# Performance work log

Hardware: AMD Instinct MI355X
Metric: run time of the kernel (lower is better)

Reference implementation:

```python
import jax, jax.numpy as jnp
import numpy as np

H = 16      # num_attention_heads
D = 128     # head_size
ROT = 32    # rotary_ndims
WIN = 256   # attention_window[layer_id]
G = 64      # max_global_tokens
BASE = 10000.0


def _rotate_half(x):
    x1, x2 = jnp.split(x, 2, axis=-1)
    return jnp.concatenate([-x2, x1], axis=-1)


def setup_inputs() -> dict:
    key = jax.random.key(0)
    ks = jax.random.split(key, 6)
    B, S, HD = 2, 2048, H * D
    hidden_states = jax.random.normal(ks[0], (B, S, HD), jnp.float32)
    attention_mask = jnp.zeros((B, 1, 1, S), jnp.float32)
    glob_idx = jnp.sort(jax.random.randint(ks[1], (B, G), 0, S), axis=-1)
    W_qkv = jax.random.normal(ks[2], (HD, 3 * HD), jnp.float32) * 0.02
    b_qkv = jnp.zeros((3 * HD,), jnp.float32)
    W_o = jax.random.normal(ks[3], (HD, HD), jnp.float32) * 0.02
    b_o = jnp.zeros((HD,), jnp.float32)
    return {"hidden_states": hidden_states, "attention_mask": attention_mask,
            "glob_idx": glob_idx, "W_qkv": W_qkv, "b_qkv": b_qkv,
            "W_o": W_o, "b_o": b_o}


def reference(hidden_states, attention_mask, glob_idx, W_qkv, b_qkv, W_o, b_o):
    B, S, HD = hidden_states.shape
    qkv = (hidden_states @ W_qkv + b_qkv).reshape(B, S, H, 3 * D)
    q = qkv[..., :D].transpose(0, 2, 1, 3)        # [B,H,S,D]
    k = qkv[..., D:2 * D].transpose(0, 2, 1, 3)
    v = qkv[..., 2 * D:].transpose(0, 2, 1, 3)

    # GPT-NeoX rotary on first ROT dims
    inv_freq = 1.0 / (BASE ** (jnp.arange(0, ROT, 2, dtype=jnp.float32) / ROT))
    freqs = jnp.einsum('s,f->sf', jnp.arange(S, dtype=jnp.float32), inv_freq)
    emb = jnp.concatenate([freqs, freqs], axis=-1)           # [S,ROT]
    cos = jnp.cos(emb)[None, None]
    sin = jnp.sin(emb)[None, None]
    q = jnp.concatenate([q[..., :ROT] * cos + _rotate_half(q[..., :ROT]) * sin,
                         q[..., ROT:]], axis=-1)
    k = jnp.concatenate([k[..., :ROT] * cos + _rotate_half(k[..., :ROT]) * sin,
                         k[..., ROT:]], axis=-1)

    # step_attn path: keys/values are head-averaged before attention (key.mean(1))
    k_mean = k.mean(axis=1)   # [B,S,D]
    v_mean = v.mean(axis=1)
    scale = 1.0 / jnp.sqrt(jnp.float32(D))
    minv = jnp.finfo(jnp.float32).min

    s0 = jnp.einsum('bhqd,bkd->bhqk', q[:, :, :WIN], k_mean[:, :WIN]) * scale
    causal = jnp.tril(jnp.ones((WIN, WIN), bool))
    s0 = jnp.where(causal[None, None], s0, minv) + attention_mask[..., :WIN]
    out0 = jnp.einsum('bhqk,bkd->bhqd', jax.nn.softmax(s0, axis=-1), v_mean[:, :WIN])

    Sq = S - WIN
    steps = jnp.arange(Sq)
    win_pos = steps[:, None] + 1 + jnp.arange(WIN)[None, :]
    k_win = k_mean[:, win_pos]
    v_win = v_mean[:, win_pos]
    mask_win = attention_mask[:, 0, 0, :][:, win_pos][:, None]
    qs = q[:, :, WIN:]                                        # [B,H,Sq,D]
    s_win = jnp.einsum('bhqd,bqwd->bhqw', qs, k_win) * scale + mask_win

    k_glob = jnp.take_along_axis(k_mean, glob_idx[..., None], axis=1)  # [B,G,D]
    v_glob = jnp.take_along_axis(v_mean, glob_idx[..., None], axis=1)
    # sorted indices: 'filter < i then truncate to G' == prefix-valid mask per slot
    valid = (glob_idx[:, None, :] < steps[None, :, None])[:, None]     # [B,1,Sq,G]
    s_glob = jnp.where(valid, jnp.einsum('bhqd,bgd->bhqg', qs, k_glob) * scale, minv)

    w = jax.nn.softmax(jnp.concatenate([s_glob, s_win], axis=-1), axis=-1)
    out_steps = (jnp.einsum('bhqg,bgd->bhqd', w[..., :G], v_glob)
                 + jnp.einsum('bhqw,bqwd->bhqd', w[..., G:], v_win))

    out = jnp.concatenate([out0, out_steps], axis=2)          # [B,H,S,D]
    out = out.transpose(0, 2, 1, 3).reshape(B, S, HD)
    return out @ W_o + b_o
```

## Files before the change

### kernel.cpp

```cpp
#include <hip/hip_runtime.h>
#include <math.h>

#define SCALE_ 0.08838834764831845f
#define MINV_  (-3.4028234663852886e38f)

typedef __bf16 bf16;
typedef bf16  bf16x4 __attribute__((ext_vector_type(4)));
typedef bf16  bf16x8 __attribute__((ext_vector_type(8)));
typedef float f32x4  __attribute__((ext_vector_type(4)));
typedef float f32x16 __attribute__((ext_vector_type(16)));
typedef float float4v __attribute__((ext_vector_type(4)));

#define LD8(p) (*(const bf16x8*)(p))

__device__ __forceinline__ f32x4 mfma16(bf16x8 a, bf16x8 b, f32x4 c) {
    return __builtin_amdgcn_mfma_f32_16x16x32_bf16(a, b, c, 0, 0, 0);
}
__device__ __forceinline__ f32x16 mfma32(bf16x8 a, bf16x8 b, f32x16 c) {
    return __builtin_amdgcn_mfma_f32_32x32x16_bf16(a, b, c, 0, 0, 0);
}

typedef const __attribute__((address_space(1))) void* gas_t;
typedef __attribute__((address_space(3))) void* sas_t;
__device__ __forceinline__ void gload_lds16(const void* g, void* l) {
    __builtin_amdgcn_global_load_lds((gas_t)g, (sas_t)l, 16, 0, 0);
}

__global__ __launch_bounds__(256) void prep_kernel(const float* __restrict__ hidden, bf16* __restrict__ A16,
                                                   const float* __restrict__ Wqkv, bf16* __restrict__ BT1,
                                                   const float* __restrict__ Wo, bf16* __restrict__ BT2,
                                                   const float* __restrict__ bqkv, float* __restrict__ bias1)
{
    int x = blockIdx.x;
    if (x < 512) {
        int k0 = x * 4;
        int j = threadIdx.x;
        float acc[4];
        #pragma unroll
        for (int k = 0; k < 4; k++) acc[k] = 0.f;
        for (int h = 0; h < 16; h++) {
            #pragma unroll
            for (int k = 0; k < 4; k++)
                acc[k] += Wqkv[(size_t)(k0 + k) * 6144 + h * 384 + 128 + j];
        }
        #pragma unroll
        for (int k = 0; k < 4; k++)
            BT1[(size_t)(2048 + j) * 2048 + k0 + k] = (bf16)(acc[k] * 0.0625f);
        return;
    }
    if (x == 512) {
        for (int c = threadIdx.x; c < 2304; c += 256) {
            if (c < 2048) bias1[c] = bqkv[(c >> 7) * 384 + (c & 127)];
            else {
                int j = c - 2048; float s = 0.f;
                for (int h = 0; h < 16; h++) s += bqkv[h * 384 + 128 + j];
                bias1[c] = s * 0.0625f;
            }
        }
        return;
    }
    if (x < 8705) {
        int i = ((x - 513) * 256 + threadIdx.x) * 4;
        float4v v = *(const float4v*)(hidden + i);
        bf16x4 o; o.x = (bf16)v.x; o.y = (bf16)v.y; o.z = (bf16)v.z; o.w = (bf16)v.w;
        *(bf16x4*)(A16 + i) = o;
        return;
    }
    __shared__ float tile[32][33];
    int t = x - 8705;
    int z = t >> 12;
    int tt = t & 4095;
    const float* W = z ? Wo : Wqkv;
    bf16* BT = z ? BT2 : BT1;
    int srcStride = z ? 2048 : 6144;
    int k0 = (tt & 63) * 32, n0 = (tt >> 6) * 32;
    int c = threadIdx.x & 31, r = threadIdx.x >> 5;
    int n = n0 + c;
    int src = z ? n : ((n >> 7) * 384 + (n & 127));
    #pragma unroll
    for (int rr = 0; rr < 32; rr += 8)
        tile[r + rr][c] = W[(size_t)(k0 + r + rr) * srcStride + src];
    __syncthreads();
    #pragma unroll
    for (int rr = 0; rr < 32; rr += 8)
        BT[(size_t)(n0 + r + rr) * 2048 + k0 + c] = (bf16)tile[c][r + rr];
}


#define GEMM64_PROLOGUE_AND_KLOOP                                                         \
    __shared__ __align__(16) bf16 As[128 * 64];                                           \
    __shared__ __align__(16) bf16 Bs[64 * 64];                                            \
    const int tid  = threadIdx.x;                                                         \
    const int wv   = tid >> 6, lane = tid & 63, l32 = lane & 31, half = lane >> 5;        \
    const int m0 = blockIdx.y * 128, n0 = blockIdx.x * 64;                                \
    int rowSA[4], colSA[4];                                                               \
    _Pragma("unroll")                                                                     \
    for (int j = 0; j < 4; j++) {                                                         \
        int flat = (wv * 4 + j) * 64 + lane;                                              \
        rowSA[j] = flat >> 3;                                                             \
        colSA[j] = ((flat & 7) ^ (rowSA[j] & 7)) * 8;                                     \
    }                                                                                     \
    int rowSB[2], colSB[2];                                                               \
    _Pragma("unroll")                                                                     \
    for (int j = 0; j < 2; j++) {                                                         \
        int flat = (wv * 2 + j) * 64 + lane;                                              \
        rowSB[j] = flat >> 3;                                                             \
        colSB[j] = ((flat & 7) ^ (rowSB[j] & 7)) * 8;                                     \
    }                                                                                     \
    f32x16 acc[2];                                                                        \
    _Pragma("unroll")                                                                     \
    for (int i = 0; i < 2; i++)                                                           \
        _Pragma("unroll")                                                                 \
        for (int r = 0; r < 16; r++) acc[i][r] = 0.f;                                     \
    for (int kk = 0; kk < K; kk += 64) {                                                  \
        __syncthreads();                                                                  \
        _Pragma("unroll")                                                                 \
        for (int j = 0; j < 4; j++)                                                       \
            gload_lds16(A  + (size_t)(m0 + rowSA[j]) * K + kk + colSA[j], &As[(wv * 4 + j) * 512]); \
        _Pragma("unroll")                                                                 \
        for (int j = 0; j < 2; j++)                                                       \
            gload_lds16(BT + (size_t)(n0 + rowSB[j]) * K + kk + colSB[j], &Bs[(wv * 2 + j) * 512]); \
        __syncthreads();                                                                  \
        bf16x8 af[4], bfr[2][4];                                                          \
        const int rowA = wv * 32 + l32;                                                   \
        _Pragma("unroll")                                                                 \
        for (int k16 = 0; k16 < 4; k16++) {                                               \
            int lc = k16 * 2 + half;                                                      \
            af[k16] = LD8(&As[rowA * 64 + ((lc ^ (rowA & 7)) * 8)]);                      \
        }                                                                                 \
        _Pragma("unroll")                                                                 \
        for (int nt = 0; nt < 2; nt++) {                                                  \
            int rowB = nt * 32 + l32;                                                     \
            _Pragma("unroll")                                                             \
            for (int k16 = 0; k16 < 4; k16++) {                                           \
                int lc = k16 * 2 + half;                                                  \
                bfr[nt][k16] = LD8(&Bs[rowB * 64 + ((lc ^ (rowB & 7)) * 8)]);             \
            }                                                                             \
        }                                                                                 \
        _Pragma("unroll")                                                                 \
        for (int k16 = 0; k16 < 4; k16++)                                                 \
            _Pragma("unroll")                                                             \
            for (int nt = 0; nt < 2; nt++)                                                \
                acc[nt] = mfma32(af[k16], bfr[nt][k16], acc[nt]);                         \
    }

__global__ __launch_bounds__(256) void gemm_rot_kernel(const bf16* __restrict__ A, const bf16* __restrict__ BT,
                                                       const float* __restrict__ bias, bf16* __restrict__ C,
                                                       int M, int N, int K)
{
    GEMM64_PROLOGUE_AND_KLOOP

    #pragma unroll
    for (int nt = 0; nt < 2; nt++) {
        int n = n0 + nt * 32 + l32;
        float bn = bias[n];
        const bool rot = ((n0 & 127) == 0) && (nt == 0) && (n0 <= 2048);
        float inv = rot ? __expf(-0.575646273248511f * (float)(l32 & 15)) : 0.f;
        #pragma unroll
        for (int r = 0; r < 16; r++) {
            int m = m0 + wv * 32 + (r & 3) + 8 * (r >> 2) + 4 * half;
            float v = acc[nt][r] + bn;
            if (rot) {
                float ang = (float)(m & 2047) * inv;
                float cs, sn;
                __sincosf(ang, &sn, &cs);
                float pv = __shfl_xor(v, 16, 64);
                v = (l32 < 16) ? (v * cs - pv * sn) : (v * cs + pv * sn);
            }
            C[(size_t)m * N + n] = (bf16)v;
        }
    }
}

__global__ __launch_bounds__(256) void gemm_out_kernel(const bf16* __restrict__ A, const bf16* __restrict__ BT,
                                                       const float* __restrict__ bias, float* __restrict__ C,
                                                       int M, int N, int K)
{
    GEMM64_PROLOGUE_AND_KLOOP

    #pragma unroll
    for (int nt = 0; nt < 2; nt++) {
        int n = n0 + nt * 32 + l32;
        float bn = bias[n];
        #pragma unroll
        for (int r = 0; r < 16; r++) {
            int m = m0 + wv * 32 + (r & 3) + 8 * (r >> 2) + 4 * half;
            C[(size_t)m * N + n] = acc[nt][r] + bn;
        }
    }
}

__global__ __launch_bounds__(256) void pretile_kernel(const bf16* __restrict__ C1, const int* __restrict__ gidx,
                                                      bf16* __restrict__ KF, bf16* __restrict__ VF)
{
    __shared__ bf16 Vt[64][130];
    const int c = blockIdx.x, b = blockIdx.y;
    const bool isGlob = (c == 32);
    const int tid = threadIdx.x;

    {
        int row = tid >> 2, cb = (tid & 3) * 32;
        int pos = isGlob ? gidx[b * 64 + row] : (c * 64 + row);
        const bf16* src = C1 + (size_t)(b * 2048 + pos) * 2304 + 2176 + cb;
        #pragma unroll
        for (int k = 0; k < 4; k++)
            *(bf16x8*)&Vt[row][cb + k * 8] = LD8(src + k * 8);
    }
    __syncthreads();

    #pragma unroll
    for (int i = 0; i < 4; i++) {
        int sid = tid + i * 256;
        int lane = sid & 63, fi = sid >> 6;
        int l16 = lane & 15, quad = lane >> 4;
        int t = fi >> 2, ks = fi & 3;
        int pos = isGlob ? gidx[b * 64 + t * 16 + l16] : (c * 64 + t * 16 + l16);
        const bf16* src = C1 + (size_t)(b * 2048 + pos) * 2304 + 2048 + ks * 32 + quad * 8;
        *(bf16x8*)&KF[((size_t)(b * 33 + c) * 16 + fi) * 512 + lane * 8] = LD8(src);
    }

    #pragma unroll
    for (int i = 0; i < 4; i++) {
        int sid = tid + i * 256;
        int lane = sid & 63, fi = sid >> 6;
        int l16 = lane & 15, quad = lane >> 4;
        int dt = fi >> 1, ks2 = fi & 1;
        int d = dt * 16 + l16;
        bf16x8 v;
        #pragma unroll
        for (int j = 0; j < 8; j++)
            v[j] = Vt[ks2 * 32 + quad * 8 + j][d];
        *(bf16x8*)&VF[((size_t)(b * 33 + c) * 16 + fi) * 512 + lane * 8] = v;
    }
}

#define PSTRIDE 88

__device__ __forceinline__ void attn0_body(int bx, int h, int b, bf16* Pw,
                                           const bf16* __restrict__ C1, const bf16* __restrict__ KF,
                                           const bf16* __restrict__ VF, const float* __restrict__ mask,
                                           bf16* __restrict__ attn)
{
    const int tid = threadIdx.x, wv = tid >> 6, lane = tid & 63, quad = lane >> 4, l16 = lane & 15;
    const int q0 = (bx * 4 + wv) * 16;

    bf16x8 af[4];
    const bf16* qbase = C1 + (size_t)(b * 2048 + q0 + l16) * 2304 + h * 128;
    #pragma unroll
    for (int ks = 0; ks < 4; ks++) af[ks] = LD8(qbase + ks * 32 + quad * 8);

    f32x4 m_run = (f32x4){MINV_, MINV_, MINV_, MINV_};
    f32x4 l_run = (f32x4){0.f, 0.f, 0.f, 0.f};
    f32x4 O[8];
    #pragma unroll
    for (int dt = 0; dt < 8; dt++) O[dt] = (f32x4){0.f, 0.f, 0.f, 0.f};

    for (int c = 0; c <= bx; c++) {
        const bf16* KFc = KF + ((size_t)(b * 33 + c) * 16) * 512;
        const bf16* VFc = VF + ((size_t)(b * 33 + c) * 16) * 512;

        f32x4 acc[4];
        #pragma unroll
        for (int t = 0; t < 4; t++) acc[t] = (f32x4){0.f, 0.f, 0.f, 0.f};
        #pragma unroll
        for (int t = 0; t < 4; t++)
            #pragma unroll
            for (int ks = 0; ks < 4; ks++)
                acc[t] = mfma16(af[ks], LD8(KFc + (size_t)(t * 4 + ks) * 512 + lane * 8), acc[t]);

        float sv[4][4];
        #pragma unroll
        for (int t = 0; t < 4; t++) {
            int key = c * 64 + t * 16 + l16;
            float addv = mask[b * 2048 + key];
            #pragma unroll
            for (int r = 0; r < 4; r++) {
                int q = q0 + quad * 4 + r;
                sv[t][r] = (key <= q) ? (acc[t][r] * SCALE_ + addv) : MINV_;
            }
        }

        f32x4 cm;
        #pragma unroll
        for (int r = 0; r < 4; r++) cm[r] = fmaxf(fmaxf(sv[0][r], sv[1][r]), fmaxf(sv[2][r], sv[3][r]));
        #pragma unroll
        for (int ms = 1; ms < 16; ms <<= 1)
            #pragma unroll
            for (int r = 0; r < 4; r++) cm[r] = fmaxf(cm[r], __shfl_xor(cm[r], ms, 64));

        f32x4 nm, alpha;
        #pragma unroll
        for (int r = 0; r < 4; r++) { nm[r] = fmaxf(m_run[r], cm[r]); alpha[r] = __expf(m_run[r] - nm[r]); }

        float pv[4][4];
        f32x4 cs = (f32x4){0.f, 0.f, 0.f, 0.f};
        #pragma unroll
        for (int t = 0; t < 4; t++)
            #pragma unroll
            for (int r = 0; r < 4; r++) {
                pv[t][r] = __expf(sv[t][r] - nm[r]);
                cs[r] += pv[t][r];
            }
        #pragma unroll
        for (int ms = 1; ms < 16; ms <<= 1)
            #pragma unroll
            for (int r = 0; r < 4; r++) cs[r] += __shfl_xor(cs[r], ms, 64);

        m_run = nm;
        #pragma unroll
        for (int r = 0; r < 4; r++) l_run[r] = l_run[r] * alpha[r] + cs[r];
        #pragma unroll
        for (int dt = 0; dt < 8; dt++)
            #pragma unroll
            for (int r = 0; r < 4; r++) O[dt][r] *= alpha[r];

        #pragma unroll
        for (int t = 0; t < 4; t++)
            #pragma unroll
            for (int r = 0; r < 4; r++)
                Pw[(quad * 4 + r) * PSTRIDE + t * 16 + l16] = (bf16)pv[t][r];
        bf16x8 pa0 = LD8(&Pw[l16 * PSTRIDE + quad * 8]);
        bf16x8 pa1 = LD8(&Pw[l16 * PSTRIDE + 32 + quad * 8]);

        #pragma unroll
        for (int dt = 0; dt < 8; dt++) {
            O[dt] = mfma16(pa0, LD8(VFc + (size_t)(dt * 2 + 0) * 512 + lane * 8), O[dt]);
            O[dt] = mfma16(pa1, LD8(VFc + (size_t)(dt * 2 + 1) * 512 + lane * 8), O[dt]);
        }
    }

    f32x4 invl;
    #pragma unroll
    for (int r = 0; r < 4; r++) invl[r] = 1.0f / l_run[r];
    #pragma unroll
    for (int dt = 0; dt < 8; dt++)
        #pragma unroll
        for (int r = 0; r < 4; r++) {
            int q = q0 + quad * 4 + r;
            attn[(size_t)(b * 2048 + q) * 2048 + h * 128 + dt * 16 + l16] = (bf16)(O[dt][r] * invl[r]);
        }
}

__device__ __forceinline__ void attn_steps_body(int sb, int b, bf16* Pw,
                                                const bf16* __restrict__ C1, const bf16* __restrict__ KF,
                                                const bf16* __restrict__ VF, const float* __restrict__ mask,
                                                const int* __restrict__ gidx, bf16* __restrict__ attn)
{
    const int tid = threadIdx.x, wv = tid >> 6, lane = tid & 63, quad = lane >> 4, l16 = lane & 15;
    const int step = sb * 4 + wv, p = 256 + step;

    bf16x8 af[4];
    const bf16* qrow = C1 + (size_t)(b * 2048 + p) * 2304;
    #pragma unroll
    for (int ks = 0; ks < 4; ks++) af[ks] = LD8(qrow + l16 * 128 + ks * 32 + quad * 8);

    int gix[4];
    #pragma unroll
    for (int t = 0; t < 4; t++) gix[t] = gidx[b * 64 + t * 16 + l16];

    f32x4 m_run = (f32x4){MINV_, MINV_, MINV_, MINV_};
    f32x4 l_run = (f32x4){0.f, 0.f, 0.f, 0.f};
    f32x4 O[8];
    #pragma unroll
    for (int dt = 0; dt < 8; dt++) O[dt] = (f32x4){0.f, 0.f, 0.f, 0.f};

    const int c0 = (step + 1) >> 6;

    for (int iter = 0; iter < 6; iter++) {
        int c;
        bool isGlob = (iter == 0);
        if (isGlob) c = 32;
        else { c = c0 + iter - 1; if (c > 31) break; }

        const bf16* KFc = KF + ((size_t)(b * 33 + c) * 16) * 512;
        const bf16* VFc = VF + ((size_t)(b * 33 + c) * 16) * 512;

        f32x4 acc[4];
        #pragma unroll
        for (int t = 0; t < 4; t++) acc[t] = (f32x4){0.f, 0.f, 0.f, 0.f};
        #pragma unroll
        for (int t = 0; t < 4; t++)
            #pragma unroll
            for (int ks = 0; ks < 4; ks++)
                acc[t] = mfma16(af[ks], LD8(KFc + (size_t)(t * 4 + ks) * 512 + lane * 8), acc[t]);

        float sv[4][4];
        bool vld[4];
        #pragma unroll
        for (int t = 0; t < 4; t++) {
            float addv = 0.f;
            if (isGlob) vld[t] = gix[t] < step;
            else {
                int pos = c * 64 + t * 16 + l16;
                vld[t] = (unsigned)(pos - step - 1) < 256u;
                addv = mask[b * 2048 + pos];
            }
            #pragma unroll
            for (int r = 0; r < 4; r++) sv[t][r] = vld[t] ? (acc[t][r] * SCALE_ + addv) : MINV_;
        }

        f32x4 cm;
        #pragma unroll
        for (int r = 0; r < 4; r++) cm[r] = fmaxf(fmaxf(sv[0][r], sv[1][r]), fmaxf(sv[2][r], sv[3][r]));
        #pragma unroll
        for (int ms = 1; ms < 16; ms <<= 1)
            #pragma unroll
            for (int r = 0; r < 4; r++) cm[r] = fmaxf(cm[r], __shfl_xor(cm[r], ms, 64));

        f32x4 nm, alpha;
        #pragma unroll
        for (int r = 0; r < 4; r++) { nm[r] = fmaxf(m_run[r], cm[r]); alpha[r] = __expf(m_run[r] - nm[r]); }

        float pv[4][4];
        f32x4 cs = (f32x4){0.f, 0.f, 0.f, 0.f};
        #pragma unroll
        for (int t = 0; t < 4; t++)
            #pragma unroll
            for (int r = 0; r < 4; r++) {
                pv[t][r] = vld[t] ? __expf(sv[t][r] - nm[r]) : 0.f;
                cs[r] += pv[t][r];
            }
        #pragma unroll
        for (int ms = 1; ms < 16; ms <<= 1)
            #pragma unroll
            for (int r = 0; r < 4; r++) cs[r] += __shfl_xor(cs[r], ms, 64);

        m_run = nm;
        #pragma unroll
        for (int r = 0; r < 4; r++) l_run[r] = l_run[r] * alpha[r] + cs[r];
        #pragma unroll
        for (int dt = 0; dt < 8; dt++)
            #pragma unroll
            for (int r = 0; r < 4; r++) O[dt][r] *= alpha[r];

        #pragma unroll
        for (int t = 0; t < 4; t++)
            #pragma unroll
            for (int r = 0; r < 4; r++)
                Pw[(quad * 4 + r) * PSTRIDE + t * 16 + l16] = (bf16)pv[t][r];
        bf16x8 pa0 = LD8(&Pw[l16 * PSTRIDE + quad * 8]);
        bf16x8 pa1 = LD8(&Pw[l16 * PSTRIDE + 32 + quad * 8]);

        #pragma unroll
        for (int dt = 0; dt < 8; dt++) {
            O[dt] = mfma16(pa0, LD8(VFc + (size_t)(dt * 2 + 0) * 512 + lane * 8), O[dt]);
            O[dt] = mfma16(pa1, LD8(VFc + (size_t)(dt * 2 + 1) * 512 + lane * 8), O[dt]);
        }
    }

    f32x4 invl;
    #pragma unroll
    for (int r = 0; r < 4; r++) invl[r] = 1.0f / l_run[r];
    #pragma unroll
    for (int dt = 0; dt < 8; dt++)
        #pragma unroll
        for (int r = 0; r < 4; r++) {
            int h = quad * 4 + r;
            attn[(size_t)(b * 2048 + p) * 2048 + h * 128 + dt * 16 + l16] = (bf16)(O[dt][r] * invl[r]);
        }
}

__global__ __launch_bounds__(256) void attn_all_kernel(const bf16* __restrict__ C1, const bf16* __restrict__ KF,
                                                       const bf16* __restrict__ VF, const float* __restrict__ mask,
                                                       const int* __restrict__ gidx, bf16* __restrict__ attn)
{
    __shared__ __align__(16) bf16 Ps[4 * 16 * PSTRIDE];
    const int wv = threadIdx.x >> 6;
    bf16* Pw = &Ps[wv * (16 * PSTRIDE)];
    if (blockIdx.x < 448) {
        attn_steps_body(blockIdx.x, blockIdx.y, Pw, C1, KF, VF, mask, gidx, attn);
    } else {
        int bi = blockIdx.x - 448;
        attn0_body(bi >> 4, bi & 15, blockIdx.y, Pw, C1, KF, VF, mask, attn);
    }
}

extern "C" void kernel_launch(void* const* d_in, const int* in_sizes, int n_in,
                              void* d_out, int out_size, void* d_ws, size_t ws_size,
                              hipStream_t stream)
{
    const float* hidden = (const float*)d_in[0];
    const float* amask  = (const float*)d_in[1];
    const int*   gidx   = (const int*)d_in[2];
    const float* Wqkv   = (const float*)d_in[3];
    const float* bqkv   = (const float*)d_in[4];
    const float* Wo     = (const float*)d_in[5];
    const float* bo     = (const float*)d_in[6];

    char* ws = (char*)d_ws;
    size_t off = 0;
    auto take = [&](size_t bytes) -> char* {
        char* p = ws + off;
        off = (off + bytes + 255) & ~(size_t)255;
        return p;
    };
    bf16*  A16   = (bf16*)take(4096ull * 2048 * 2);
    bf16*  BT1   = (bf16*)take(2304ull * 2048 * 2);
    bf16*  BT2   = (bf16*)take(2048ull * 2048 * 2);
    bf16*  C1    = (bf16*)take(4096ull * 2304 * 2);
    bf16*  KF    = (bf16*)take(2ull * 33 * 16 * 512 * 2);
    bf16*  VF    = (bf16*)take(2ull * 33 * 16 * 512 * 2);
    bf16*  attnb = (bf16*)take(4096ull * 2048 * 2);
    float* bias1 = (float*)take(2304 * 4);

    prep_kernel<<<16897, 256, 0, stream>>>(hidden, A16, Wqkv, BT1, Wo, BT2, bqkv, bias1);

    gemm_rot_kernel<<<dim3(36, 32), 256, 0, stream>>>(A16, BT1, bias1, C1, 4096, 2304, 2048);

    pretile_kernel<<<dim3(33, 2), 256, 0, stream>>>(C1, gidx, KF, VF);

    attn_all_kernel<<<dim3(512, 2), 256, 0, stream>>>(C1, KF, VF, amask, gidx, attnb);

    gemm_out_kernel<<<dim3(32, 32), 256, 0, stream>>>(attnb, BT2, bo, (float*)d_out, 4096, 2048, 2048);

    (void)in_sizes; (void)n_in; (void)out_size; (void)ws_size;
}
```

Before: 298.6 us.

## Double-buffer LDS tiles in QKV and output GEMM k-loops

Converts the shared GEMM k-loop to a two-stage double-buffered pipeline: tiles t and t+1 are prefetched into separate LDS buffers, and the loop waits on partial vmcnt before computing on the current buffer, then issues the load for t+2. This overlaps global-to-LDS transfer with MFMA compute instead of serializing load, barrier and compute each iteration. It doubles LDS use per block, which may reduce occupancy, and relies on hand-placed waitcnt and barriers being correct.

```diff
diff --git a/kernel.cpp b/kernel.cpp
--- a/kernel.cpp
+++ b/kernel.cpp
@@ -87,9 +87,9 @@
 }
 
 
-#define GEMM64_PROLOGUE_AND_KLOOP                                                         \
-    __shared__ __align__(16) bf16 As[128 * 64];                                           \
-    __shared__ __align__(16) bf16 Bs[64 * 64];                                            \
+#define GEMM64DB_PROLOGUE_AND_KLOOP                                                       \
+    __shared__ __align__(16) bf16 As[2][128 * 64];                                        \
+    __shared__ __align__(16) bf16 Bs[2][64 * 64];                                         \
     const int tid  = threadIdx.x;                                                         \
     const int wv   = tid >> 6, lane = tid & 63, l32 = lane & 31, half = lane >> 5;        \
     const int m0 = blockIdx.y * 128, n0 = blockIdx.x * 64;                                \
@@ -107,48 +107,63 @@
         rowSB[j] = flat >> 3;                                                             \
         colSB[j] = ((flat & 7) ^ (rowSB[j] & 7)) * 8;                                     \
     }                                                                                     \
+    const int ktiles = K >> 6;                                                            \
+    auto stage = [&](int t, int bsel) {          \
+        int kk = t << 6;                                                                  \
+        _Pragma("unroll")                                                                 \
+        for (int j = 0; j < 4; j++)                                                       \
+            gload_lds16(A  + (size_t)(m0 + rowSA[j]) * K + kk + colSA[j], &As[bsel][(wv * 4 + j) * 512]); \
+        _Pragma("unroll")                                                                 \
+        for (int j = 0; j < 2; j++)                                                       \
+            gload_lds16(BT + (size_t)(n0 + rowSB[j]) * K + kk + colSB[j], &Bs[bsel][(wv * 2 + j) * 512]); \
+    };                                                                                    \
     f32x16 acc[2];                                                                        \
     _Pragma("unroll")                                                                     \
     for (int i = 0; i < 2; i++)                                                           \
         _Pragma("unroll")                                                                 \
         for (int r = 0; r < 16; r++) acc[i][r] = 0.f;                                     \
-    for (int kk = 0; kk < K; kk += 64) {                                                  \
-        __syncthreads();                                                                  \
-        _Pragma("unroll")                                                                 \
-        for (int j = 0; j < 4; j++)                                                       \
-            gload_lds16(A  + (size_t)(m0 + rowSA[j]) * K + kk + colSA[j], &As[(wv * 4 + j) * 512]); \
-        _Pragma("unroll")                                                                 \
-        for (int j = 0; j < 2; j++)                                                       \
-            gload_lds16(BT + (size_t)(n0 + rowSB[j]) * K + kk + colSB[j], &Bs[(wv * 2 + j) * 512]); \
-        __syncthreads();                                                                  \
+    stage(0, 0);                                                                          \
+    stage(1, 1);                                                                          \
+    for (int t = 0; t < ktiles; ++t) {                                                    \
+        const int cur = t & 1;                                                            \
+        if (t < ktiles - 1) asm volatile("s_waitcnt vmcnt(6)" ::: "memory");              \
+        else                asm volatile("s_waitcnt vmcnt(0)" ::: "memory");              \
+        __builtin_amdgcn_s_barrier();                                                     \
+        asm volatile("" ::: "memory");                                                    \
+        const bf16* Ab = &As[cur][0];                                                     \
+        const bf16* Bb = &Bs[cur][0];                                                     \
         bf16x8 af[4], bfr[2][4];                                                          \
         const int rowA = wv * 32 + l32;                                                   \
         _Pragma("unroll")                                                                 \
         for (int k16 = 0; k16 < 4; k16++) {                                               \
             int lc = k16 * 2 + half;                                                      \
-            af[k16] = LD8(&As[rowA * 64 + ((lc ^ (rowA & 7)) * 8)]);                      \
+            af[k16] = LD8(&Ab[rowA * 64 + ((lc ^ (rowA & 7)) * 8)]);                      \
         }                                                                                 \
         _Pragma("unroll")                                                                 \
-        for (int nt = 0; nt < 2; nt++) {                                                  \
-            int rowB = nt * 32 + l32;                                                     \
+        for (int nt2 = 0; nt2 < 2; nt2++) {                                               \
+            int rowB = nt2 * 32 + l32;                                                    \
             _Pragma("unroll")                                                             \
             for (int k16 = 0; k16 < 4; k16++) {                                           \
                 int lc = k16 * 2 + half;                                                  \
-                bfr[nt][k16] = LD8(&Bs[rowB * 64 + ((lc ^ (rowB & 7)) * 8)]);             \
+                bfr[nt2][k16] = LD8(&Bb[rowB * 64 + ((lc ^ (rowB & 7)) * 8)]);            \
             }                                                                             \
         }                                                                                 \
         _Pragma("unroll")                                                                 \
         for (int k16 = 0; k16 < 4; k16++)                                                 \
             _Pragma("unroll")                                                             \
-            for (int nt = 0; nt < 2; nt++)                                                \
-                acc[nt] = mfma32(af[k16], bfr[nt][k16], acc[nt]);                         \
+            for (int nt2 = 0; nt2 < 2; nt2++)                                             \
+                acc[nt2] = mfma32(af[k16], bfr[nt2][k16], acc[nt2]);                      \
+        asm volatile("" ::: "memory");                                                    \
+        __builtin_amdgcn_s_barrier();                                                     \
+        asm volatile("" ::: "memory");                                                    \
+        if (t + 2 < ktiles) stage(t + 2, cur);                                            \
     }
 
 __global__ __launch_bounds__(256) void gemm_rot_kernel(const bf16* __restrict__ A, const bf16* __restrict__ BT,
                                                        const float* __restrict__ bias, bf16* __restrict__ C,
                                                        int M, int N, int K)
 {
-    GEMM64_PROLOGUE_AND_KLOOP
+    GEMM64DB_PROLOGUE_AND_KLOOP
 
     #pragma unroll
     for (int nt = 0; nt < 2; nt++) {
@@ -176,7 +191,7 @@
                                                        const float* __restrict__ bias, float* __restrict__ C,
                                                        int M, int N, int K)
 {
-    GEMM64_PROLOGUE_AND_KLOOP
+    GEMM64DB_PROLOGUE_AND_KLOOP
 
     #pragma unroll
     for (int nt = 0; nt < 2; nt++) {
```

New measurement: 318.3 us. 1.07x slower.
